# Optimization experiments

Measured on AMD Instinct MI355X. Metric: run time of the kernel, lower is better.

The kernel has to match this reference:

```python
import jax, jax.numpy as jnp
import numpy as np

DIM = 192
RC = 16
M = 64
LN_EPS = 1e-5
NORM_EPS = 1e-12


def _layernorm(x, g, b):
    mu = jnp.mean(x, axis=-1, keepdims=True)
    var = jnp.mean((x - mu) ** 2, axis=-1, keepdims=True)
    return (x - mu) / jnp.sqrt(var + LN_EPS) * g + b


def _l2norm(x):
    n = jnp.sqrt(jnp.sum(x * x, axis=-1, keepdims=True))
    return x / jnp.maximum(n, NORM_EPS)


def setup_inputs() -> dict:
    key = jax.random.key(0)
    ks = jax.random.split(key, 12)
    B, N = 8, 16384
    s_q = 1.0 / np.sqrt(DIM)
    inp = {
        "x": jax.random.normal(ks[0], (B, N, DIM), jnp.float32),
        "dict_tokens": jax.random.normal(ks[1], (B, M, DIM), jnp.float32),
        "H": 128,
        "W": 128,
        "wq_w": jax.random.normal(ks[2], (DIM, RC), jnp.float32) * s_q,
        "wq_b": jnp.zeros((RC,), jnp.float32),
        "wk_w": jax.random.normal(ks[3], (DIM, RC), jnp.float32) * s_q,
        "wk_b": jnp.zeros((RC,), jnp.float32),
        "wv_w": jax.random.normal(ks[4], (DIM, DIM), jnp.float32) * s_q,
        "wv_b": jnp.zeros((DIM,), jnp.float32),
        "qn_g": jnp.ones((RC,), jnp.float32),
        "qn_b": jnp.zeros((RC,), jnp.float32),
        "kn_g": jnp.ones((RC,), jnp.float32),
        "kn_b": jnp.zeros((RC,), jnp.float32),
        "conv_w": jax.random.normal(ks[5], (DIM, 1, 3, 3), jnp.float32) / 3.0,
        "conv_b": jnp.zeros((DIM,), jnp.float32),
        "temperature": jnp.ones((1,), jnp.float32),
    }
    return inp


def reference(x, dict_tokens, H, W, wq_w, wq_b, wk_w, wk_b, wv_w, wv_b,
              qn_g, qn_b, kn_g, kn_b, conv_w, conv_b, temperature):
    # q: (B,N,rc), k: (B,M,rc)
    q = _l2norm(_layernorm(x @ wq_w + wq_b, qn_g, qn_b))
    k = _l2norm(_layernorm(dict_tokens @ wk_w + wk_b, kn_g, kn_b))
    # cosine-similarity attention with clamped temperature
    attn = jnp.einsum("bnr,bmr->bnm", q, k) / jnp.maximum(temperature, 0.5)
    attn = jax.nn.softmax(attn, axis=-1)
    # value + depthwise-conv refinement over the M token axis (Mx1 image)
    v = dict_tokens @ wv_w + wv_b                       # (B,M,C)
    v_img = jnp.transpose(v, (0, 2, 1))[..., None]      # (B,C,M,1)
    v_img = jax.lax.conv_general_dilated(
        v_img, conv_w, window_strides=(1, 1), padding=((1, 1), (1, 1)),
        dimension_numbers=("NCHW", "OIHW", "NCHW"), feature_group_count=DIM)
    v_img = v_img + conv_b[None, :, None, None]
    v_img = jax.nn.gelu(v_img, approximate=False)
    v = jnp.transpose(v_img[..., 0], (0, 2, 1))         # (B,M,C)
    out = jnp.einsum("bnm,bmc->bnc", attn, v)           # (B,N,C)
    return out, attn
```

## Files before the change

kernel.cpp:

```cpp
#include <hip/hip_runtime.h>
#include <math.h>

#define B_   8
#define N_   16384
#define M_   64
#define C_   192
#define RC_  16

__global__ __launch_bounds__(256) void k_v_kernel(
    const float* __restrict__ dict, const float* __restrict__ wv_w,
    const float* __restrict__ wv_b, float* __restrict__ ws_v)
{
    const int idx = blockIdx.x * 256 + threadIdx.x;
    const int c   = idx % C_;
    const int row = idx / C_;
    const float* dr = dict + row * C_;
    float acc = wv_b[c];
    #pragma unroll 4
    for (int d = 0; d < C_; ++d)
        acc = fmaf(dr[d], wv_w[d * C_ + c], acc);
    ws_v[idx] = acc;
}

__global__ __launch_bounds__(256) void k_k_kernel(
    const float* __restrict__ dict, const float* __restrict__ wk_w,
    const float* __restrict__ wk_b, const float* __restrict__ kn_g,
    const float* __restrict__ kn_b, float* __restrict__ ws_k)
{
    const int b  = blockIdx.x;
    const int m  = threadIdx.x >> 2;
    const int j4 = threadIdx.x & 3;
    const int c0 = j4 * 4;
    const float* dr = dict + (b * M_ + m) * C_;

    float a0 = wk_b[c0+0], a1 = wk_b[c0+1], a2 = wk_b[c0+2], a3 = wk_b[c0+3];
    #pragma unroll 4
    for (int d4 = 0; d4 < C_/4; ++d4) {
        const float4 xv = ((const float4*)dr)[d4];
        const float4 w0 = *(const float4*)&wk_w[(d4*4+0)*RC_ + c0];
        const float4 w1 = *(const float4*)&wk_w[(d4*4+1)*RC_ + c0];
        const float4 w2 = *(const float4*)&wk_w[(d4*4+2)*RC_ + c0];
        const float4 w3 = *(const float4*)&wk_w[(d4*4+3)*RC_ + c0];
        a0 = fmaf(xv.x, w0.x, a0); a1 = fmaf(xv.x, w0.y, a1); a2 = fmaf(xv.x, w0.z, a2); a3 = fmaf(xv.x, w0.w, a3);
        a0 = fmaf(xv.y, w1.x, a0); a1 = fmaf(xv.y, w1.y, a1); a2 = fmaf(xv.y, w1.z, a2); a3 = fmaf(xv.y, w1.w, a3);
        a0 = fmaf(xv.z, w2.x, a0); a1 = fmaf(xv.z, w2.y, a1); a2 = fmaf(xv.z, w2.z, a2); a3 = fmaf(xv.z, w2.w, a3);
        a0 = fmaf(xv.w, w3.x, a0); a1 = fmaf(xv.w, w3.y, a1); a2 = fmaf(xv.w, w3.z, a2); a3 = fmaf(xv.w, w3.w, a3);
    }
    float s  = a0 + a1 + a2 + a3;
    float ss = a0*a0 + a1*a1 + a2*a2 + a3*a3;
    s  += __shfl_xor(s, 1);  s  += __shfl_xor(s, 2);
    ss += __shfl_xor(ss, 1); ss += __shfl_xor(ss, 2);
    const float mu   = s * (1.0f/16.0f);
    const float var  = ss * (1.0f/16.0f) - mu*mu;
    const float rstd = rsqrtf(var + 1e-5f);
    const float4 g4 = *(const float4*)&kn_g[c0];
    const float4 b4 = *(const float4*)&kn_b[c0];
    float y0 = (a0 - mu) * rstd * g4.x + b4.x;
    float y1 = (a1 - mu) * rstd * g4.y + b4.y;
    float y2 = (a2 - mu) * rstd * g4.z + b4.z;
    float y3 = (a3 - mu) * rstd * g4.w + b4.w;
    float n2 = y0*y0 + y1*y1 + y2*y2 + y3*y3;
    n2 += __shfl_xor(n2, 1); n2 += __shfl_xor(n2, 2);
    const float inv = 1.0f / fmaxf(sqrtf(n2), 1e-12f);
    float4 o; o.x = y0*inv; o.y = y1*inv; o.z = y2*inv; o.w = y3*inv;
    *(float4*)&ws_k[(b * M_ + m) * RC_ + c0] = o;
}

__global__ __launch_bounds__(256) void k_conv_kernel(
    const float* __restrict__ ws_v, const float* __restrict__ conv_w,
    const float* __restrict__ conv_b, float* __restrict__ ws_vg)
{
    const int idx = blockIdx.x * 256 + threadIdx.x;
    const int c   = idx % C_;
    const int m   = (idx / C_) % M_;
    const float ctr = ws_v[idx];
    const float up  = (m > 0)      ? ws_v[idx - C_] : 0.0f;
    const float dn  = (m < M_ - 1) ? ws_v[idx + C_] : 0.0f;
    const float w0 = conv_w[c*9 + 1];
    const float w1 = conv_w[c*9 + 4];
    const float w2 = conv_w[c*9 + 7];
    float t = conv_b[c];
    t = fmaf(up, w0, t); t = fmaf(ctr, w1, t); t = fmaf(dn, w2, t);
    ws_vg[idx] = 0.5f * t * (1.0f + erff(t * 0.70710678118654752f));
}

__global__ __launch_bounds__(256, 2) void k_main_kernel(
    const float* __restrict__ x, const float* __restrict__ ws_k,
    const float* __restrict__ ws_vg,
    const float* __restrict__ wq_w, const float* __restrict__ wq_b,
    const float* __restrict__ qn_g, const float* __restrict__ qn_b,
    const float* __restrict__ temp,
    float* __restrict__ out, float* __restrict__ attn_out)
{
    __shared__ float vg_s[M_ * C_];
    __shared__ float attn_s[M_ * 68];
    __shared__ float q_s[M_ * 20];
    __shared__ float k_s[M_ * RC_];

    const int tid = threadIdx.x;
    const int b   = blockIdx.x >> 8;
    const int n0  = (blockIdx.x & 255) * M_;

    {
        const float4* src = (const float4*)(ws_vg + b * (M_ * C_));
        float4*       dst = (float4*)vg_s;
        #pragma unroll
        for (int i = 0; i < 12; ++i)
            dst[tid + 256 * i] = src[tid + 256 * i];
        ((float4*)k_s)[tid] = ((const float4*)(ws_k + b * (M_ * RC_)))[tid];
    }

    const int r  = tid >> 2;
    const int j4 = tid & 3;
    const int c0 = j4 * 4;

    const float* xr = x + (size_t)(b * N_ + n0 + r) * C_;
    float a0 = wq_b[c0+0], a1 = wq_b[c0+1], a2 = wq_b[c0+2], a3 = wq_b[c0+3];
    #pragma unroll 4
    for (int d4 = 0; d4 < C_/4; ++d4) {
        const float4 xv = ((const float4*)xr)[d4];
        const float4 w0 = *(const float4*)&wq_w[(d4*4+0)*RC_ + c0];
        const float4 w1 = *(const float4*)&wq_w[(d4*4+1)*RC_ + c0];
        const float4 w2 = *(const float4*)&wq_w[(d4*4+2)*RC_ + c0];
        const float4 w3 = *(const float4*)&wq_w[(d4*4+3)*RC_ + c0];
        a0 = fmaf(xv.x, w0.x, a0); a1 = fmaf(xv.x, w0.y, a1); a2 = fmaf(xv.x, w0.z, a2); a3 = fmaf(xv.x, w0.w, a3);
        a0 = fmaf(xv.y, w1.x, a0); a1 = fmaf(xv.y, w1.y, a1); a2 = fmaf(xv.y, w1.z, a2); a3 = fmaf(xv.y, w1.w, a3);
        a0 = fmaf(xv.z, w2.x, a0); a1 = fmaf(xv.z, w2.y, a1); a2 = fmaf(xv.z, w2.z, a2); a3 = fmaf(xv.z, w2.w, a3);
        a0 = fmaf(xv.w, w3.x, a0); a1 = fmaf(xv.w, w3.y, a1); a2 = fmaf(xv.w, w3.z, a2); a3 = fmaf(xv.w, w3.w, a3);
    }
    {
        float s  = a0 + a1 + a2 + a3;
        float ss = a0*a0 + a1*a1 + a2*a2 + a3*a3;
        s  += __shfl_xor(s, 1);  s  += __shfl_xor(s, 2);
        ss += __shfl_xor(ss, 1); ss += __shfl_xor(ss, 2);
        const float mu   = s * (1.0f/16.0f);
        const float var  = ss * (1.0f/16.0f) - mu*mu;
        const float rstd = rsqrtf(var + 1e-5f);
        const float4 g4 = *(const float4*)&qn_g[c0];
        const float4 b4 = *(const float4*)&qn_b[c0];
        const float y0 = (a0 - mu) * rstd * g4.x + b4.x;
        const float y1 = (a1 - mu) * rstd * g4.y + b4.y;
        const float y2 = (a2 - mu) * rstd * g4.z + b4.z;
        const float y3 = (a3 - mu) * rstd * g4.w + b4.w;
        float n2 = y0*y0 + y1*y1 + y2*y2 + y3*y3;
        n2 += __shfl_xor(n2, 1); n2 += __shfl_xor(n2, 2);
        const float inv = 1.0f / fmaxf(sqrtf(n2), 1e-12f);
        float4 o; o.x = y0*inv; o.y = y1*inv; o.z = y2*inv; o.w = y3*inv;
        *(float4*)&q_s[r*20 + c0] = o;
    }

    __syncthreads();

    {
        const float tinv = 1.0f / fmaxf(temp[0], 0.5f);
        const float4 q0 = *(const float4*)&q_s[r*20 + 0];
        const float4 q1 = *(const float4*)&q_s[r*20 + 4];
        const float4 q2 = *(const float4*)&q_s[r*20 + 8];
        const float4 q3 = *(const float4*)&q_s[r*20 + 12];
        float sc[16];
        #pragma unroll
        for (int mm = 0; mm < 16; ++mm) {
            const int m = j4*16 + mm;
            const float4 k0 = *(const float4*)&k_s[m*RC_ + 0];
            const float4 k1 = *(const float4*)&k_s[m*RC_ + 4];
            const float4 k2 = *(const float4*)&k_s[m*RC_ + 8];
            const float4 k3 = *(const float4*)&k_s[m*RC_ + 12];
            float d = q0.x*k0.x;
            d = fmaf(q0.y, k0.y, d); d = fmaf(q0.z, k0.z, d); d = fmaf(q0.w, k0.w, d);
            d = fmaf(q1.x, k1.x, d); d = fmaf(q1.y, k1.y, d); d = fmaf(q1.z, k1.z, d); d = fmaf(q1.w, k1.w, d);
            d = fmaf(q2.x, k2.x, d); d = fmaf(q2.y, k2.y, d); d = fmaf(q2.z, k2.z, d); d = fmaf(q2.w, k2.w, d);
            d = fmaf(q3.x, k3.x, d); d = fmaf(q3.y, k3.y, d); d = fmaf(q3.z, k3.z, d); d = fmaf(q3.w, k3.w, d);
            sc[mm] = d * tinv;
        }
        float mx = sc[0];
        #pragma unroll
        for (int mm = 1; mm < 16; ++mm) mx = fmaxf(mx, sc[mm]);
        mx = fmaxf(mx, __shfl_xor(mx, 1)); mx = fmaxf(mx, __shfl_xor(mx, 2));
        float es = 0.0f;
        #pragma unroll
        for (int mm = 0; mm < 16; ++mm) { sc[mm] = expf(sc[mm] - mx); es += sc[mm]; }
        es += __shfl_xor(es, 1); es += __shfl_xor(es, 2);
        const float einv = 1.0f / es;
        float* aw = attn_out + (size_t)(b * N_ + n0 + r) * M_ + j4*16;
        #pragma unroll
        for (int mq = 0; mq < 4; ++mq) {
            float4 av;
            av.x = sc[mq*4+0]*einv; av.y = sc[mq*4+1]*einv;
            av.z = sc[mq*4+2]*einv; av.w = sc[mq*4+3]*einv;
            *(float4*)&attn_s[r*68 + j4*16 + mq*4] = av;
            ((float4*)aw)[mq] = av;
        }
    }

    __syncthreads();

    {
        float4 acc[12];
        #pragma unroll
        for (int cc = 0; cc < 12; ++cc) { acc[cc].x = 0.f; acc[cc].y = 0.f; acc[cc].z = 0.f; acc[cc].w = 0.f; }
        for (int m = 0; m < M_; ++m) {
            const float a = attn_s[r*68 + m];
            #pragma unroll
            for (int cc = 0; cc < 12; ++cc) {
                const float4 v = *(const float4*)&vg_s[m*C_ + cc*16 + c0];
                acc[cc].x = fmaf(a, v.x, acc[cc].x);
                acc[cc].y = fmaf(a, v.y, acc[cc].y);
                acc[cc].z = fmaf(a, v.z, acc[cc].z);
                acc[cc].w = fmaf(a, v.w, acc[cc].w);
            }
        }
        float* orow = out + (size_t)(b * N_ + n0 + r) * C_;
        #pragma unroll
        for (int cc = 0; cc < 12; ++cc)
            *(float4*)&orow[cc*16 + c0] = acc[cc];
    }
}

extern "C" void kernel_launch(void* const* d_in, const int* in_sizes, int n_in,
                              void* d_out, int out_size, void* d_ws, size_t ws_size,
                              hipStream_t stream) {
    const float* x      = (const float*)d_in[0];
    const float* dict   = (const float*)d_in[1];
    const float* wq_w   = (const float*)d_in[4];
    const float* wq_b   = (const float*)d_in[5];
    const float* wk_w   = (const float*)d_in[6];
    const float* wk_b   = (const float*)d_in[7];
    const float* wv_w   = (const float*)d_in[8];
    const float* wv_b   = (const float*)d_in[9];
    const float* qn_g   = (const float*)d_in[10];
    const float* qn_b   = (const float*)d_in[11];
    const float* kn_g   = (const float*)d_in[12];
    const float* kn_b   = (const float*)d_in[13];
    const float* conv_w = (const float*)d_in[14];
    const float* conv_b = (const float*)d_in[15];
    const float* temp   = (const float*)d_in[16];

    float* out  = (float*)d_out;
    float* attn = out + (size_t)B_ * N_ * C_;

    float* ws_v  = (float*)d_ws;
    float* ws_vg = ws_v  + B_ * M_ * C_;
    float* ws_k  = ws_vg + B_ * M_ * C_;

    k_v_kernel   <<<B_ * M_ * C_ / 256, 256, 0, stream>>>(dict, wv_w, wv_b, ws_v);
    k_k_kernel   <<<B_,                 256, 0, stream>>>(dict, wk_w, wk_b, kn_g, kn_b, ws_k);
    k_conv_kernel<<<B_ * M_ * C_ / 256, 256, 0, stream>>>(ws_v, conv_w, conv_b, ws_vg);
    k_main_kernel<<<B_ * (N_ / M_),     256, 0, stream>>>(x, ws_k, ws_vg, wq_w, wq_b,
                                                          qn_g, qn_b, temp, out, attn);
}
```

Measured before the change: 351.0 us.

## Use split-fp16 MFMA for attn@V and fuse prep kernels into one

Replaces the scalar FP32 attn@V loop with MFMA 16x16x32 f16 instructions. Precision is kept by splitting both operands into hi and scaled lo fp16 parts and doing three cross products. The V/K/conv preprocessing kernels are merged into one prep kernel that writes a transposed fp16 hi/lo V. The main kernel no longer stages the 48KB V tile in LDS, which allows four blocks per SM. The risks are extra precision error from the split approximation and B operands now read straight from global memory.

```diff
diff --git a/kernel.cpp b/kernel.cpp
--- a/kernel.cpp
+++ b/kernel.cpp
@@ -7,108 +7,138 @@
 #define C_   192
 #define RC_  16
 
-__global__ __launch_bounds__(256) void k_v_kernel(
+typedef __attribute__((ext_vector_type(8))) _Float16 f16x8;
+typedef __attribute__((ext_vector_type(4))) float    f32x4;
+typedef unsigned int   u32;
+typedef unsigned short u16;
+
+#define LO_SCALE     2048.0f
+#define LO_SCALE_INV (1.0f / 2048.0f)
+
+__global__ __launch_bounds__(256) void k_prep(
     const float* __restrict__ dict, const float* __restrict__ wv_w,
-    const float* __restrict__ wv_b, float* __restrict__ ws_v)
+    const float* __restrict__ wv_b, const float* __restrict__ conv_w,
+    const float* __restrict__ conv_b,
+    const float* __restrict__ wk_w, const float* __restrict__ wk_b,
+    const float* __restrict__ kn_g, const float* __restrict__ kn_b,
+    _Float16* __restrict__ vgt_hi, _Float16* __restrict__ vgt_lo,
+    float* __restrict__ ws_k)
 {
-    const int idx = blockIdx.x * 256 + threadIdx.x;
-    const int c   = idx % C_;
-    const int row = idx / C_;
-    const float* dr = dict + row * C_;
-    float acc = wv_b[c];
+    __shared__ float dict_s[M_ * C_];
+    __shared__ float vloc[M_ * 40];
+
+    const int t  = threadIdx.x;
+    const int b  = blockIdx.x / 6;
+    const int sl = blockIdx.x % 6;
+
+    {
+        const float4* src = (const float4*)(dict + (size_t)b * M_ * C_);
+        float4*       dst = (float4*)dict_s;
+        #pragma unroll
+        for (int i = 0; i < 12; ++i) dst[t + 256 * i] = src[t + 256 * i];
+    }
+    __syncthreads();
+
+    const int m  = t >> 2;
+    const int cg = (t & 3) * 8;
+    const int c0 = sl * 32 + cg;
+
+    float acc[8];
+    #pragma unroll
+    for (int j = 0; j < 8; ++j) acc[j] = wv_b[c0 + j];
     #pragma unroll 4
-    for (int d = 0; d < C_; ++d)
-        acc = fmaf(dr[d], wv_w[d * C_ + c], acc);
-    ws_v[idx] = acc;
+    for (int d = 0; d < C_; ++d) {
+        const float  xd = dict_s[m * C_ + d];
+        const float4 wA = *(const float4*)&wv_w[d * C_ + c0];
+        const float4 wB = *(const float4*)&wv_w[d * C_ + c0 + 4];
+        acc[0] = fmaf(xd, wA.x, acc[0]); acc[1] = fmaf(xd, wA.y, acc[1]);
+        acc[2] = fmaf(xd, wA.z, acc[2]); acc[3] = fmaf(xd, wA.w, acc[3]);
+        acc[4] = fmaf(xd, wB.x, acc[4]); acc[5] = fmaf(xd, wB.y, acc[5]);
+        acc[6] = fmaf(xd, wB.z, acc[6]); acc[7] = fmaf(xd, wB.w, acc[7]);
+    }
+    {
+        float4 a0; a0.x = acc[0]; a0.y = acc[1]; a0.z = acc[2]; a0.w = acc[3];
+        float4 a1; a1.x = acc[4]; a1.y = acc[5]; a1.z = acc[6]; a1.w = acc[7];
+        *(float4*)&vloc[m * 40 + cg]     = a0;
+        *(float4*)&vloc[m * 40 + cg + 4] = a1;
+    }
+    __syncthreads();
+
+    #pragma unroll
+    for (int j = 0; j < 8; ++j) {
+        const int   c   = c0 + j;
+        const float ctr = vloc[m * 40 + cg + j];
+        const float up  = (m > 0)      ? vloc[(m - 1) * 40 + cg + j] : 0.0f;
+        const float dn  = (m < M_ - 1) ? vloc[(m + 1) * 40 + cg + j] : 0.0f;
+        const float w0 = conv_w[c * 9 + 1];
+        const float w1 = conv_w[c * 9 + 4];
+        const float w2 = conv_w[c * 9 + 7];
+        float v = conv_b[c];
+        v = fmaf(up, w0, v); v = fmaf(ctr, w1, v); v = fmaf(dn, w2, v);
+        const float g = 0.5f * v * (1.0f + erff(v * 0.70710678118654752f));
+        const _Float16 gh = (_Float16)g;
+        const _Float16 gl = (_Float16)((g - (float)gh) * LO_SCALE);
+        const size_t o = ((size_t)b * C_ + c) * M_ + m;
+        vgt_hi[o] = gh;
+        vgt_lo[o] = gl;
+    }
+
+    if (sl == 0) {
+        const int j4  = t & 3;
+        const int c0k = j4 * 4;
+        const float* dr = dict_s + m * C_;
+        float a0 = wk_b[c0k+0], a1 = wk_b[c0k+1], a2 = wk_b[c0k+2], a3 = wk_b[c0k+3];
+        #pragma unroll 4
+        for (int d4 = 0; d4 < C_/4; ++d4) {
+            const float4 xv = *(const float4*)&dr[d4 * 4];
+            const float4 w0 = *(const float4*)&wk_w[(d4*4+0)*RC_ + c0k];
+            const float4 w1 = *(const float4*)&wk_w[(d4*4+1)*RC_ + c0k];
+            const float4 w2 = *(const float4*)&wk_w[(d4*4+2)*RC_ + c0k];
+            const float4 w3 = *(const float4*)&wk_w[(d4*4+3)*RC_ + c0k];
+            a0 = fmaf(xv.x, w0.x, a0); a1 = fmaf(xv.x, w0.y, a1); a2 = fmaf(xv.x, w0.z, a2); a3 = fmaf(xv.x, w0.w, a3);
+            a0 = fmaf(xv.y, w1.x, a0); a1 = fmaf(xv.y, w1.y, a1); a2 = fmaf(xv.y, w1.z, a2); a3 = fmaf(xv.y, w1.w, a3);
+            a0 = fmaf(xv.z, w2.x, a0); a1 = fmaf(xv.z, w2.y, a1); a2 = fmaf(xv.z, w2.z, a2); a3 = fmaf(xv.z, w2.w, a3);
+            a0 = fmaf(xv.w, w3.x, a0); a1 = fmaf(xv.w, w3.y, a1); a2 = fmaf(xv.w, w3.z, a2); a3 = fmaf(xv.w, w3.w, a3);
+        }
+        float s  = a0 + a1 + a2 + a3;
+        float ss = a0*a0 + a1*a1 + a2*a2 + a3*a3;
+        s  += __shfl_xor(s, 1);  s  += __shfl_xor(s, 2);
+        ss += __shfl_xor(ss, 1); ss += __shfl_xor(ss, 2);
+        const float mu   = s * (1.0f/16.0f);
+        const float var  = ss * (1.0f/16.0f) - mu*mu;
+        const float rstd = rsqrtf(var + 1e-5f);
+        const float4 g4 = *(const float4*)&kn_g[c0k];
+        const float4 b4 = *(const float4*)&kn_b[c0k];
+        const float y0 = (a0 - mu) * rstd * g4.x + b4.x;
+        const float y1 = (a1 - mu) * rstd * g4.y + b4.y;
+        const float y2 = (a2 - mu) * rstd * g4.z + b4.z;
+        const float y3 = (a3 - mu) * rstd * g4.w + b4.w;
+        float n2 = y0*y0 + y1*y1 + y2*y2 + y3*y3;
+        n2 += __shfl_xor(n2, 1); n2 += __shfl_xor(n2, 2);
+        const float inv = 1.0f / fmaxf(sqrtf(n2), 1e-12f);
+        float4 o; o.x = y0*inv; o.y = y1*inv; o.z = y2*inv; o.w = y3*inv;
+        *(float4*)&ws_k[((size_t)b * M_ + m) * RC_ + c0k] = o;
+    }
 }
 
-__global__ __launch_bounds__(256) void k_k_kernel(
-    const float* __restrict__ dict, const float* __restrict__ wk_w,
-    const float* __restrict__ wk_b, const float* __restrict__ kn_g,
-    const float* __restrict__ kn_b, float* __restrict__ ws_k)
-{
-    const int b  = blockIdx.x;
-    const int m  = threadIdx.x >> 2;
-    const int j4 = threadIdx.x & 3;
-    const int c0 = j4 * 4;
-    const float* dr = dict + (b * M_ + m) * C_;
-
-    float a0 = wk_b[c0+0], a1 = wk_b[c0+1], a2 = wk_b[c0+2], a3 = wk_b[c0+3];
-    #pragma unroll 4
-    for (int d4 = 0; d4 < C_/4; ++d4) {
-        const float4 xv = ((const float4*)dr)[d4];
-        const float4 w0 = *(const float4*)&wk_w[(d4*4+0)*RC_ + c0];
-        const float4 w1 = *(const float4*)&wk_w[(d4*4+1)*RC_ + c0];
-        const float4 w2 = *(const float4*)&wk_w[(d4*4+2)*RC_ + c0];
-        const float4 w3 = *(const float4*)&wk_w[(d4*4+3)*RC_ + c0];
-        a0 = fmaf(xv.x, w0.x, a0); a1 = fmaf(xv.x, w0.y, a1); a2 = fmaf(xv.x, w0.z, a2); a3 = fmaf(xv.x, w0.w, a3);
-        a0 = fmaf(xv.y, w1.x, a0); a1 = fmaf(xv.y, w1.y, a1); a2 = fmaf(xv.y, w1.z, a2); a3 = fmaf(xv.y, w1.w, a3);
-        a0 = fmaf(xv.z, w2.x, a0); a1 = fmaf(xv.z, w2.y, a1); a2 = fmaf(xv.z, w2.z, a2); a3 = fmaf(xv.z, w2.w, a3);
-        a0 = fmaf(xv.w, w3.x, a0); a1 = fmaf(xv.w, w3.y, a1); a2 = fmaf(xv.w, w3.z, a2); a3 = fmaf(xv.w, w3.w, a3);
-    }
-    float s  = a0 + a1 + a2 + a3;
-    float ss = a0*a0 + a1*a1 + a2*a2 + a3*a3;
-    s  += __shfl_xor(s, 1);  s  += __shfl_xor(s, 2);
-    ss += __shfl_xor(ss, 1); ss += __shfl_xor(ss, 2);
-    const float mu   = s * (1.0f/16.0f);
-    const float var  = ss * (1.0f/16.0f) - mu*mu;
-    const float rstd = rsqrtf(var + 1e-5f);
-    const float4 g4 = *(const float4*)&kn_g[c0];
-    const float4 b4 = *(const float4*)&kn_b[c0];
-    float y0 = (a0 - mu) * rstd * g4.x + b4.x;
-    float y1 = (a1 - mu) * rstd * g4.y + b4.y;
-    float y2 = (a2 - mu) * rstd * g4.z + b4.z;
-    float y3 = (a3 - mu) * rstd * g4.w + b4.w;
-    float n2 = y0*y0 + y1*y1 + y2*y2 + y3*y3;
-    n2 += __shfl_xor(n2, 1); n2 += __shfl_xor(n2, 2);
-    const float inv = 1.0f / fmaxf(sqrtf(n2), 1e-12f);
-    float4 o; o.x = y0*inv; o.y = y1*inv; o.z = y2*inv; o.w = y3*inv;
-    *(float4*)&ws_k[(b * M_ + m) * RC_ + c0] = o;
-}
-
-__global__ __launch_bounds__(256) void k_conv_kernel(
-    const float* __restrict__ ws_v, const float* __restrict__ conv_w,
-    const float* __restrict__ conv_b, float* __restrict__ ws_vg)
-{
-    const int idx = blockIdx.x * 256 + threadIdx.x;
-    const int c   = idx % C_;
-    const int m   = (idx / C_) % M_;
-    const float ctr = ws_v[idx];
-    const float up  = (m > 0)      ? ws_v[idx - C_] : 0.0f;
-    const float dn  = (m < M_ - 1) ? ws_v[idx + C_] : 0.0f;
-    const float w0 = conv_w[c*9 + 1];
-    const float w1 = conv_w[c*9 + 4];
-    const float w2 = conv_w[c*9 + 7];
-    float t = conv_b[c];
-    t = fmaf(up, w0, t); t = fmaf(ctr, w1, t); t = fmaf(dn, w2, t);
-    ws_vg[idx] = 0.5f * t * (1.0f + erff(t * 0.70710678118654752f));
-}
-
-__global__ __launch_bounds__(256, 2) void k_main_kernel(
+__global__ __launch_bounds__(256, 4) void k_main_kernel(
     const float* __restrict__ x, const float* __restrict__ ws_k,
-    const float* __restrict__ ws_vg,
+    const _Float16* __restrict__ vgt_hi, const _Float16* __restrict__ vgt_lo,
     const float* __restrict__ wq_w, const float* __restrict__ wq_b,
     const float* __restrict__ qn_g, const float* __restrict__ qn_b,
     const float* __restrict__ temp,
     float* __restrict__ out, float* __restrict__ attn_out)
 {
-    __shared__ float vg_s[M_ * C_];
-    __shared__ float attn_s[M_ * 68];
     __shared__ float q_s[M_ * 20];
     __shared__ float k_s[M_ * RC_];
+    __shared__ __attribute__((aligned(16))) _Float16 ahi_s[M_ * 72];
+    __shared__ __attribute__((aligned(16))) _Float16 alo_s[M_ * 72];
 
     const int tid = threadIdx.x;
     const int b   = blockIdx.x >> 8;
     const int n0  = (blockIdx.x & 255) * M_;
 
-    {
-        const float4* src = (const float4*)(ws_vg + b * (M_ * C_));
-        float4*       dst = (float4*)vg_s;
-        #pragma unroll
-        for (int i = 0; i < 12; ++i)
-            dst[tid + 256 * i] = src[tid + 256 * i];
-        ((float4*)k_s)[tid] = ((const float4*)(ws_k + b * (M_ * RC_)))[tid];
-    }
+    ((float4*)k_s)[tid] = ((const float4*)(ws_k + (size_t)b * M_ * RC_))[tid];
 
     const int r  = tid >> 2;
     const int j4 = tid & 3;
@@ -169,7 +199,7 @@
             d = fmaf(q0.y, k0.y, d); d = fmaf(q0.z, k0.z, d); d = fmaf(q0.w, k0.w, d);
             d = fmaf(q1.x, k1.x, d); d = fmaf(q1.y, k1.y, d); d = fmaf(q1.z, k1.z, d); d = fmaf(q1.w, k1.w, d);
             d = fmaf(q2.x, k2.x, d); d = fmaf(q2.y, k2.y, d); d = fmaf(q2.z, k2.z, d); d = fmaf(q2.w, k2.w, d);
-            d = fmaf(q3.x, k3.x, d); d = fmaf(q3.y, k3.y, d); d = fmaf(q3.z, k3.z, d); d = fmaf(q3.w, k3.w, d);
+            d = fmaf(q3.x, k3.x, d); d = fmaf(q3.y, k3.y, d); d = fmaf(q3.w, k3.w, d); d = fmaf(q3.z, k3.z, d);
             sc[mm] = d * tinv;
         }
         float mx = sc[0];
@@ -181,38 +211,70 @@
         for (int mm = 0; mm < 16; ++mm) { sc[mm] = expf(sc[mm] - mx); es += sc[mm]; }
         es += __shfl_xor(es, 1); es += __shfl_xor(es, 2);
         const float einv = 1.0f / es;
+        #pragma unroll
+        for (int mm = 0; mm < 16; ++mm) sc[mm] *= einv;
+
         float* aw = attn_out + (size_t)(b * N_ + n0 + r) * M_ + j4*16;
         #pragma unroll
         for (int mq = 0; mq < 4; ++mq) {
             float4 av;
-            av.x = sc[mq*4+0]*einv; av.y = sc[mq*4+1]*einv;
-            av.z = sc[mq*4+2]*einv; av.w = sc[mq*4+3]*einv;
-            *(float4*)&attn_s[r*68 + j4*16 + mq*4] = av;
+            av.x = sc[mq*4+0]; av.y = sc[mq*4+1]; av.z = sc[mq*4+2]; av.w = sc[mq*4+3];
             ((float4*)aw)[mq] = av;
         }
+        f16x8 h0v, h1v, l0v, l1v;
+        #pragma unroll
+        for (int i = 0; i < 8; ++i) {
+            const _Float16 ha = (_Float16)sc[i];
+            h0v[i] = ha;
+            l0v[i] = (_Float16)((sc[i] - (float)ha) * LO_SCALE);
+            const _Float16 hb = (_Float16)sc[i + 8];
+            h1v[i] = hb;
+            l1v[i] = (_Float16)((sc[i + 8] - (float)hb) * LO_SCALE);
+        }
+        *(f16x8*)&ahi_s[r*72 + j4*16]     = h0v;
+        *(f16x8*)&ahi_s[r*72 + j4*16 + 8] = h1v;
+        *(f16x8*)&alo_s[r*72 + j4*16]     = l0v;
+        *(f16x8*)&alo_s[r*72 + j4*16 + 8] = l1v;
     }
 
     __syncthreads();
 
     {
-        float4 acc[12];
-        #pragma unroll
-        for (int cc = 0; cc < 12; ++cc) { acc[cc].x = 0.f; acc[cc].y = 0.f; acc[cc].z = 0.f; acc[cc].w = 0.f; }
-        for (int m = 0; m < M_; ++m) {
-            const float a = attn_s[r*68 + m];
+        const int w    = tid >> 6;
+        const int lane = tid & 63;
+        const int n16  = lane & 15;
+        const int g    = lane >> 4;
+        const int gr   = w * 16 + n16;
+
+        const f16x8 Ah0 = *(const f16x8*)&ahi_s[gr*72 +      8*g];
+        const f16x8 Ah1 = *(const f16x8*)&ahi_s[gr*72 + 32 + 8*g];
+        const f16x8 Al0 = *(const f16x8*)&alo_s[gr*72 +      8*g];
+        const f16x8 Al1 = *(const f16x8*)&alo_s[gr*72 + 32 + 8*g];
+
+        const _Float16* bh = vgt_hi + ((size_t)b * C_ + n16) * M_ + 8*g;
+        const _Float16* bl = vgt_lo + ((size_t)b * C_ + n16) * M_ + 8*g;
+
+        float* obase = out + (size_t)(b * N_ + n0 + w*16 + 4*g) * C_ + n16;
+
+        #pragma unroll
+        for (int nt = 0; nt < 12; ++nt) {
+            const int off = nt * 16 * M_;
+            const f16x8 Bh0 = *(const f16x8*)(bh + off);
+            const f16x8 Bl0 = *(const f16x8*)(bl + off);
+            const f16x8 Bh1 = *(const f16x8*)(bh + off + 32);
+            const f16x8 Bl1 = *(const f16x8*)(bl + off + 32);
+            f32x4 acc0 = (f32x4)(0.0f);
+            f32x4 acc1 = (f32x4)(0.0f);
+            acc0 = __builtin_amdgcn_mfma_f32_16x16x32_f16(Ah0, Bh0, acc0, 0, 0, 0);
+            acc0 = __builtin_amdgcn_mfma_f32_16x16x32_f16(Ah1, Bh1, acc0, 0, 0, 0);
+            acc1 = __builtin_amdgcn_mfma_f32_16x16x32_f16(Ah0, Bl0, acc1, 0, 0, 0);
+            acc1 = __builtin_amdgcn_mfma_f32_16x16x32_f16(Al0, Bh0, acc1, 0, 0, 0);
+            acc1 = __builtin_amdgcn_mfma_f32_16x16x32_f16(Ah1, Bl1, acc1, 0, 0, 0);
+            acc1 = __builtin_amdgcn_mfma_f32_16x16x32_f16(Al1, Bh1, acc1, 0, 0, 0);
             #pragma unroll
-            for (int cc = 0; cc < 12; ++cc) {
-                const float4 v = *(const float4*)&vg_s[m*C_ + cc*16 + c0];
-                acc[cc].x = fmaf(a, v.x, acc[cc].x);
-                acc[cc].y = fmaf(a, v.y, acc[cc].y);
-                acc[cc].z = fmaf(a, v.z, acc[cc].z);
-                acc[cc].w = fmaf(a, v.w, acc[cc].w);
-            }
-        }
-        float* orow = out + (size_t)(b * N_ + n0 + r) * C_;
-        #pragma unroll
-        for (int cc = 0; cc < 12; ++cc)
-            *(float4*)&orow[cc*16 + c0] = acc[cc];
+            for (int rg = 0; rg < 4; ++rg)
+                obase[(size_t)rg * C_ + nt*16] = acc0[rg] + acc1[rg] * LO_SCALE_INV;
+        }
     }
 }
 
@@ -238,13 +300,14 @@
     float* out  = (float*)d_out;
     float* attn = out + (size_t)B_ * N_ * C_;
 
-    float* ws_v  = (float*)d_ws;
-    float* ws_vg = ws_v  + B_ * M_ * C_;
-    float* ws_k  = ws_vg + B_ * M_ * C_;
-
-    k_v_kernel   <<<B_ * M_ * C_ / 256, 256, 0, stream>>>(dict, wv_w, wv_b, ws_v);
-    k_k_kernel   <<<B_,                 256, 0, stream>>>(dict, wk_w, wk_b, kn_g, kn_b, ws_k);
-    k_conv_kernel<<<B_ * M_ * C_ / 256, 256, 0, stream>>>(ws_v, conv_w, conv_b, ws_vg);
-    k_main_kernel<<<B_ * (N_ / M_),     256, 0, stream>>>(x, ws_k, ws_vg, wq_w, wq_b,
-                                                          qn_g, qn_b, temp, out, attn);
+    float*    ws_k   = (float*)d_ws;
+    _Float16* vgt_hi = (_Float16*)(ws_k + (size_t)B_ * M_ * RC_);
+    _Float16* vgt_lo = vgt_hi + (size_t)B_ * C_ * M_;
+
+    k_prep<<<B_ * 6, 256, 0, stream>>>(dict, wv_w, wv_b, conv_w, conv_b,
+                                       wk_w, wk_b, kn_g, kn_b,
+                                       vgt_hi, vgt_lo, ws_k);
+    k_main_kernel<<<B_ * (N_ / M_), 256, 0, stream>>>(x, ws_k, vgt_hi, vgt_lo,
+                                                      wq_w, wq_b, qn_g, qn_b,
+                                                      temp, out, attn);
 }
```

After: 355.9 us. Within noise of the previous version (+1.4%).
